# Performance work log

Hardware: AMD Instinct MI355X
Metric: run time of the kernel (lower is better)

## Reference

```python
import jax, jax.numpy as jnp
import numpy as np

B, N, F_IN, F_OUT = 8, 2048, 64, 64
ALPHA = 0.2
NEG = -9e15


def setup_inputs() -> dict:
    key = jax.random.key(0)
    k1, k2, k3, k4 = jax.random.split(key, 4)
    h = jax.random.normal(k1, (B, N, F_IN), dtype=jnp.float32)
    adj = jax.random.randint(k2, (N, N), 0, 2).astype(jnp.float32)
    W = jax.random.normal(k3, (F_OUT, F_IN), dtype=jnp.float32) * 0.05
    a = jax.random.normal(k4, (2 * F_OUT,), dtype=jnp.float32) * 0.05
    return {"h": h, "adj": adj, "W": W, "a": a}


def reference(h, adj, W, a):
    # Wh = h @ W^T  : [B, N, F_OUT]
    Wh = jnp.einsum("bnf,of->bno", h, W)
    # a([Wh_i, Wh_j]) decomposes exactly into a1.Wh_i + a2.Wh_j
    e1 = Wh @ a[:F_OUT]          # [B, N] contribution of source node i
    e2 = Wh @ a[F_OUT:]          # [B, N] contribution of target node j
    e = jax.nn.leaky_relu(e1[:, :, None] + e2[:, None, :], negative_slope=ALPHA)
    att = jnp.where(adj[None, :, :] > 0, e, NEG)
    att = jax.nn.softmax(att, axis=-1)   # [B, N, N]
    h_prime = jnp.einsum("bij,bjo->bio", att, Wh)
    return jax.nn.elu(h_prime)
```

## Files before the change

### kernel.cpp

```cpp
#include <hip/hip_runtime.h>
#include <hip/hip_bf16.h>
#include <math.h>


#define NN 2048
#define BB 8

typedef __attribute__((ext_vector_type(8))) short s8v;
typedef __attribute__((ext_vector_type(4))) float f4v;
typedef __attribute__((ext_vector_type(16))) float f16v;
typedef __attribute__((ext_vector_type(4))) unsigned u4v;

static __device__ __forceinline__ unsigned pk_bf16(float lo, float hi) {
  __hip_bfloat162 t = __float22bfloat162_rn(float2{lo, hi});
  return *(unsigned*)&t;
}
static __device__ __forceinline__ unsigned short bf16rne(float x) {
  union { float f; unsigned u; } c; c.f = x;
  unsigned r = c.u + 0x7FFFu + ((c.u >> 16) & 1u);
  return (unsigned short)(r >> 16);
}

__global__ __launch_bounds__(256, 2) void k_pre(
    const float* __restrict__ adj, const float* __restrict__ h,
    const float* __restrict__ W, const float* __restrict__ a,
    unsigned long long* __restrict__ adjq, unsigned short* __restrict__ whswz,
    float2* __restrict__ e1pn, unsigned* __restrict__ e2pk) {
  const int t = threadIdx.x, lane = t & 63, w = t >> 6;

  if (blockIdx.x >= 512) {
    const int bid = blockIdx.x - 512;
    const int row = bid * 2 + (w >> 1);
    const int half = w & 1;
    const float* ar = adj + (size_t)row * NN + half * 1024;
    unsigned long long* aq = adjq + row * 32 + half * 16;
    #pragma unroll
    for (int it = 0; it < 16; ++it) {
      unsigned long long m = __ballot(ar[it * 64 + lane] > 0.f);
      if (lane == 0) aq[it] = m;
    }
    return;
  }

  __shared__ __align__(16) float hs[32][68];
  const int rowBase = blockIdx.x * 32;
  const int b = rowBase >> 11, n0 = rowBase & (NN - 1);

  float wr[64];
  #pragma unroll
  for (int k = 0; k < 16; ++k)
    *(f4v*)&wr[k * 4] = *(const f4v*)&W[lane * 64 + k * 4];

  #pragma unroll
  for (int qq = 0; qq < 2; ++qq) {
    const int idx = t + 256 * qq;
    const int r = idx >> 4, c = (idx & 15) * 4;
    *(f4v*)&hs[r][c] = *(const f4v*)&h[(size_t)(rowBase + r) * 64 + c];
  }
  const float a1v = a[lane], a2v = a[64 + lane];
  __syncthreads();

  const int r0 = w * 8;
  float acc[8];
  #pragma unroll
  for (int rr = 0; rr < 8; ++rr) acc[rr] = 0.f;
  #pragma unroll
  for (int f4i = 0; f4i < 16; ++f4i) {
    f4v hv[8];
    #pragma unroll
    for (int rr = 0; rr < 8; ++rr)
      hv[rr] = *(const f4v*)&hs[r0 + rr][f4i * 4];
    #pragma unroll
    for (int x = 0; x < 4; ++x) {
      const float wv = wr[f4i * 4 + x];
      #pragma unroll
      for (int rr = 0; rr < 8; ++rr) acc[rr] = fmaf(hv[rr][x], wv, acc[rr]);
    }
  }

  {
    union { s8v v; unsigned u[4]; } cv;
    cv.u[0] = pk_bf16(acc[0], acc[1]);
    cv.u[1] = pk_bf16(acc[2], acc[3]);
    cv.u[2] = pk_bf16(acc[4], acc[5]);
    cv.u[3] = pk_bf16(acc[6], acc[7]);
    const int jc = (n0 + w * 8) >> 4;
    const int oh = lane >> 5;
    const int lp = ((w & 1) << 5) + (lane & 31);
    unsigned short* dst = whswz + ((size_t)b << 17) + (jc << 10) + (oh << 9) + (lp << 3);
    *(s8v*)dst = cv.v;
  }

  float s1[8], s2[8];
  #pragma unroll
  for (int rr = 0; rr < 8; ++rr) { s1[rr] = acc[rr] * a1v; s2[rr] = acc[rr] * a2v; }
  #pragma unroll
  for (int m = 1; m < 64; m <<= 1)
    #pragma unroll
    for (int rr = 0; rr < 8; ++rr) {
      s1[rr] += __shfl_xor(s1[rr], m);
      s2[rr] += __shfl_xor(s2[rr], m);
    }
  #pragma unroll
  for (int rr = 0; rr < 8; ++rr) {
    if (lane == 0) {
      e1pn[rowBase + rr + r0] = float2{__expf(s1[rr]), __expf(0.2f * s1[rr])};
      e2pk[rowBase + rr + r0] =
          (unsigned)bf16rne(__expf(s2[rr])) |
          ((unsigned)bf16rne(__expf(0.2f * s2[rr])) << 16);
    }
  }
}

__global__ __launch_bounds__(512, 4) void k_attn(
    const unsigned long long* __restrict__ adjq,
    const unsigned short* __restrict__ whswz,
    const float2* __restrict__ e1png, const unsigned* __restrict__ e2pkg,
    float* __restrict__ out) {
  union SM {
    unsigned e2bf[NN];
    float pc[8][32][68];
  };
  __shared__ __align__(16) SM sm;
  __shared__ float ls[8][32];

  const int t = threadIdx.x, lane = t & 63, w = t >> 6;
  const int m32 = lane & 31, kh = lane >> 5;
  const int g = blockIdx.x;
  const int b = g & 7;
  const int i0 = (g >> 3) << 5;
  const size_t bN = (size_t)b * NN;

  ((u4v*)sm.e2bf)[t] = ((const u4v*)(e2pkg + bN))[t];

  const float2 e1f = e1png[bN + i0 + m32];
  const float E1p = e1f.x, E1n = e1f.y;
  const unsigned long long* arow = adjq + (size_t)(i0 + m32) * 32 + w * 4;
  const unsigned short* wb = whswz + ((size_t)b << 17);

  f16v acc0, acc1;
  #pragma unroll
  for (int r = 0; r < 16; ++r) { acc0[r] = 0.f; acc1[r] = 0.f; }
  float psum = 0.f;

  auto pgen = [&](u4v e0, u4v e1, unsigned bits) -> s8v {
    float p[8];
    #pragma unroll
    for (int e = 0; e < 8; ++e) {
      const unsigned dw = e < 4 ? e0[e] : e1[e - 4];
      const float E2p = __uint_as_float(dw << 16);
      const float E2n = __uint_as_float(dw & 0xffff0000u);
      const float mp = E1p * E2p;
      const float mn = E1n * E2n;
      float pv = mp > 1.f ? mp : mn;
      pv = ((bits >> e) & 1u) ? pv : 0.f;
      psum += pv;
      p[e] = pv;
    }
    union { s8v v; unsigned u[4]; } cv;
    cv.u[0] = pk_bf16(p[0], p[1]);
    cv.u[1] = pk_bf16(p[2], p[3]);
    cv.u[2] = pk_bf16(p[4], p[5]);
    cv.u[3] = pk_bf16(p[6], p[7]);
    return cv.v;
  };

  __syncthreads();

  unsigned long long am = 0;
  #pragma unroll
  for (int it = 0; it < 8; ++it) {
    const int jcl = it * 2;
    const int jcA = w * 16 + jcl, jcB = jcA + 1;
    const s8v bA0 = *(const s8v*)(wb + (jcA << 10) + (lane << 3));
    const s8v bA1 = *(const s8v*)(wb + (jcA << 10) + 512 + (lane << 3));
    const s8v bB0 = *(const s8v*)(wb + (jcB << 10) + (lane << 3));
    const s8v bB1 = *(const s8v*)(wb + (jcB << 10) + 512 + (lane << 3));
    if ((it & 1) == 0) am = arow[it >> 1];
    const u4v eA0 = *(const u4v*)&sm.e2bf[(jcA << 4) + (kh << 3)];
    const u4v eA1 = *(const u4v*)&sm.e2bf[(jcA << 4) + (kh << 3) + 4];
    const u4v eB0 = *(const u4v*)&sm.e2bf[(jcB << 4) + (kh << 3)];
    const u4v eB1 = *(const u4v*)&sm.e2bf[(jcB << 4) + (kh << 3) + 4];

    const unsigned bitsA = (unsigned)(am >> (((jcl)&3) * 16 + kh * 8)) & 0xffu;
    const unsigned bitsB = (unsigned)(am >> (((jcl + 1) & 3) * 16 + kh * 8)) & 0xffu;
    const s8v afA = pgen(eA0, eA1, bitsA);
    const s8v afB = pgen(eB0, eB1, bitsB);

    acc0 = __builtin_amdgcn_mfma_f32_32x32x16_bf16(afA, bA0, acc0, 0, 0, 0);
    acc1 = __builtin_amdgcn_mfma_f32_32x32x16_bf16(afA, bA1, acc1, 0, 0, 0);
    acc0 = __builtin_amdgcn_mfma_f32_32x32x16_bf16(afB, bB0, acc0, 0, 0, 0);
    acc1 = __builtin_amdgcn_mfma_f32_32x32x16_bf16(afB, bB1, acc1, 0, 0, 0);
  }

  psum += __shfl_xor(psum, 32);
  __syncthreads();
  if (lane < 32) ls[w][lane] = psum;
  #pragma unroll
  for (int r = 0; r < 16; ++r) {
    const int row = (r & 3) + 8 * (r >> 2) + 4 * kh;
    sm.pc[w][row][m32] = acc0[r];
    sm.pc[w][row][32 + m32] = acc1[r];
  }
  __syncthreads();

  const int row = t >> 4, c0 = (t & 15) * 4;
  f4v sum = *(const f4v*)&sm.pc[0][row][c0];
  #pragma unroll
  for (int j = 1; j < 8; ++j) sum += *(const f4v*)&sm.pc[j][row][c0];
  float rsum = ls[0][row];
  #pragma unroll
  for (int j = 1; j < 8; ++j) rsum += ls[j][row];
  f4v o;
  #pragma unroll
  for (int x = 0; x < 4; ++x) {
    float v = sum[x] / rsum;
    o[x] = v > 0.f ? v : expm1f(v);
  }
  *(f4v*)&out[(bN + i0 + row) * 64 + c0] = o;
}

extern "C" void kernel_launch(void* const* d_in, const int* in_sizes, int n_in,
                              void* d_out, int out_size, void* d_ws, size_t ws_size,
                              hipStream_t stream) {
  (void)in_sizes; (void)n_in; (void)out_size; (void)ws_size;
  const float* h   = (const float*)d_in[0];
  const float* adj = (const float*)d_in[1];
  const float* W   = (const float*)d_in[2];
  const float* a   = (const float*)d_in[3];
  float* outp = (float*)d_out;

  unsigned short* whswz = (unsigned short*)d_ws;
  float2* e1pn = (float2*)((char*)d_ws + (size_t)BB * 64 * NN * 2);
  unsigned* e2pk = (unsigned*)(e1pn + (size_t)BB * NN);
  unsigned long long* adjq = (unsigned long long*)(e2pk + (size_t)BB * NN);

  k_pre<<<1536, 256, 0, stream>>>(adj, h, W, a, adjq, whswz, e1pn, e2pk);
  k_attn<<<512, 512, 0, stream>>>(adjq, whswz, e1pn, e2pk, outp);
}
```

Baseline: 97.88 us.

## Halve attention block to 4 waves with 4-deep prefetched Wh ring

The attention kernel now runs 4 waves per block instead of 8, so each wave handles 32 j-chunks instead of 16. The wave loads all its adjacency bits up front and keeps Wh tiles in a 4-stage register ring, issuing each global load four iterations before the matching MFMA. It also splits the row-sum into two accumulators and shrinks the cross-wave reduction buffer. The cost is half as many threads in flight per block, more registers per wave and a longer serial loop per wave.

```diff
diff --git a/kernel.cpp b/kernel.cpp
--- a/kernel.cpp
+++ b/kernel.cpp
@@ -10,6 +10,7 @@
 typedef __attribute__((ext_vector_type(4))) float f4v;
 typedef __attribute__((ext_vector_type(16))) float f16v;
 typedef __attribute__((ext_vector_type(4))) unsigned u4v;
+typedef __attribute__((ext_vector_type(2))) unsigned long long u64v2;
 
 static __device__ __forceinline__ unsigned pk_bf16(float lo, float hi) {
   __hip_bfloat162 t = __float22bfloat162_rn(float2{lo, hi});
@@ -112,17 +113,17 @@
   }
 }
 
-__global__ __launch_bounds__(512, 4) void k_attn(
+__global__ __launch_bounds__(256, 2) void k_attn(
     const unsigned long long* __restrict__ adjq,
     const unsigned short* __restrict__ whswz,
     const float2* __restrict__ e1png, const unsigned* __restrict__ e2pkg,
     float* __restrict__ out) {
   union SM {
     unsigned e2bf[NN];
-    float pc[8][32][68];
+    float pc[4][32][68];
   };
   __shared__ __align__(16) SM sm;
-  __shared__ float ls[8][32];
+  __shared__ float ls[4][32];
 
   const int t = threadIdx.x, lane = t & 63, w = t >> 6;
   const int m32 = lane & 31, kh = lane >> 5;
@@ -132,18 +133,40 @@
   const size_t bN = (size_t)b * NN;
 
   ((u4v*)sm.e2bf)[t] = ((const u4v*)(e2pkg + bN))[t];
+  ((u4v*)sm.e2bf)[t + 256] = ((const u4v*)(e2pkg + bN))[t + 256];
 
   const float2 e1f = e1png[bN + i0 + m32];
   const float E1p = e1f.x, E1n = e1f.y;
-  const unsigned long long* arow = adjq + (size_t)(i0 + m32) * 32 + w * 4;
-  const unsigned short* wb = whswz + ((size_t)b << 17);
+
+  const unsigned long long* arow = adjq + (size_t)(i0 + m32) * 32 + w * 8;
+  unsigned long long am[8];
+  #pragma unroll
+  for (int qq = 0; qq < 4; ++qq)
+    *(u64v2*)&am[qq * 2] = *(const u64v2*)(arow + qq * 2);
+
+  const unsigned short* wb = whswz + ((size_t)b << 17) + ((size_t)(w * 32) << 10);
 
   f16v acc0, acc1;
   #pragma unroll
   for (int r = 0; r < 16; ++r) { acc0[r] = 0.f; acc1[r] = 0.f; }
-  float psum = 0.f;
-
-  auto pgen = [&](u4v e0, u4v e1, unsigned bits) -> s8v {
+  float psA = 0.f, psB = 0.f;
+
+  s8v buf[4][2];
+  #pragma unroll
+  for (int k = 0; k < 4; ++k) {
+    buf[k][0] = *(const s8v*)(wb + (k << 10) + (lane << 3));
+    buf[k][1] = *(const s8v*)(wb + (k << 10) + 512 + (lane << 3));
+  }
+
+  __syncthreads();
+
+  #pragma unroll 4
+  for (int k = 0; k < 32; ++k) {
+    const int x = k & 3;
+    const int eb = ((w * 32 + k) << 4) + (kh << 3);
+    const u4v e0 = *(const u4v*)&sm.e2bf[eb];
+    const u4v e1 = *(const u4v*)&sm.e2bf[eb + 4];
+    const unsigned bits = (unsigned)(am[k >> 2] >> ((k & 3) * 16 + kh * 8)) & 0xffu;
     float p[8];
     #pragma unroll
     for (int e = 0; e < 8; ++e) {
@@ -154,45 +177,34 @@
       const float mn = E1n * E2n;
       float pv = mp > 1.f ? mp : mn;
       pv = ((bits >> e) & 1u) ? pv : 0.f;
-      psum += pv;
       p[e] = pv;
     }
-    union { s8v v; unsigned u[4]; } cv;
-    cv.u[0] = pk_bf16(p[0], p[1]);
-    cv.u[1] = pk_bf16(p[2], p[3]);
-    cv.u[2] = pk_bf16(p[4], p[5]);
-    cv.u[3] = pk_bf16(p[6], p[7]);
-    return cv.v;
-  };
-
-  __syncthreads();
-
-  unsigned long long am = 0;
-  #pragma unroll
-  for (int it = 0; it < 8; ++it) {
-    const int jcl = it * 2;
-    const int jcA = w * 16 + jcl, jcB = jcA + 1;
-    const s8v bA0 = *(const s8v*)(wb + (jcA << 10) + (lane << 3));
-    const s8v bA1 = *(const s8v*)(wb + (jcA << 10) + 512 + (lane << 3));
-    const s8v bB0 = *(const s8v*)(wb + (jcB << 10) + (lane << 3));
-    const s8v bB1 = *(const s8v*)(wb + (jcB << 10) + 512 + (lane << 3));
-    if ((it & 1) == 0) am = arow[it >> 1];
-    const u4v eA0 = *(const u4v*)&sm.e2bf[(jcA << 4) + (kh << 3)];
-    const u4v eA1 = *(const u4v*)&sm.e2bf[(jcA << 4) + (kh << 3) + 4];
-    const u4v eB0 = *(const u4v*)&sm.e2bf[(jcB << 4) + (kh << 3)];
-    const u4v eB1 = *(const u4v*)&sm.e2bf[(jcB << 4) + (kh << 3) + 4];
-
-    const unsigned bitsA = (unsigned)(am >> (((jcl)&3) * 16 + kh * 8)) & 0xffu;
-    const unsigned bitsB = (unsigned)(am >> (((jcl + 1) & 3) * 16 + kh * 8)) & 0xffu;
-    const s8v afA = pgen(eA0, eA1, bitsA);
-    const s8v afB = pgen(eB0, eB1, bitsB);
-
-    acc0 = __builtin_amdgcn_mfma_f32_32x32x16_bf16(afA, bA0, acc0, 0, 0, 0);
-    acc1 = __builtin_amdgcn_mfma_f32_32x32x16_bf16(afA, bA1, acc1, 0, 0, 0);
-    acc0 = __builtin_amdgcn_mfma_f32_32x32x16_bf16(afB, bB0, acc0, 0, 0, 0);
-    acc1 = __builtin_amdgcn_mfma_f32_32x32x16_bf16(afB, bB1, acc1, 0, 0, 0);
-  }
-
+    {
+      const float s01 = p[0] + p[1], s23 = p[2] + p[3];
+      const float s45 = p[4] + p[5], s67 = p[6] + p[7];
+      if (k & 1) psB += (s01 + s23) + (s45 + s67);
+      else       psA += (s01 + s23) + (s45 + s67);
+    }
+    s8v af;
+    {
+      union { s8v v; unsigned u[4]; } cv;
+      cv.u[0] = pk_bf16(p[0], p[1]);
+      cv.u[1] = pk_bf16(p[2], p[3]);
+      cv.u[2] = pk_bf16(p[4], p[5]);
+      cv.u[3] = pk_bf16(p[6], p[7]);
+      af = cv.v;
+    }
+
+    acc0 = __builtin_amdgcn_mfma_f32_32x32x16_bf16(af, buf[x][0], acc0, 0, 0, 0);
+    acc1 = __builtin_amdgcn_mfma_f32_32x32x16_bf16(af, buf[x][1], acc1, 0, 0, 0);
+
+    if (k < 28) {
+      buf[x][0] = *(const s8v*)(wb + ((k + 4) << 10) + (lane << 3));
+      buf[x][1] = *(const s8v*)(wb + ((k + 4) << 10) + 512 + (lane << 3));
+    }
+  }
+
+  float psum = psA + psB;
   psum += __shfl_xor(psum, 32);
   __syncthreads();
   if (lane < 32) ls[w][lane] = psum;
@@ -204,20 +216,26 @@
   }
   __syncthreads();
 
-  const int row = t >> 4, c0 = (t & 15) * 4;
-  f4v sum = *(const f4v*)&sm.pc[0][row][c0];
-  #pragma unroll
-  for (int j = 1; j < 8; ++j) sum += *(const f4v*)&sm.pc[j][row][c0];
-  float rsum = ls[0][row];
-  #pragma unroll
-  for (int j = 1; j < 8; ++j) rsum += ls[j][row];
-  f4v o;
-  #pragma unroll
-  for (int x = 0; x < 4; ++x) {
-    float v = sum[x] / rsum;
-    o[x] = v > 0.f ? v : expm1f(v);
-  }
-  *(f4v*)&out[(bN + i0 + row) * 64 + c0] = o;
+  const int row = t >> 3, c0 = (t & 7) * 8;
+  f4v s0 = *(const f4v*)&sm.pc[0][row][c0];
+  f4v s1 = *(const f4v*)&sm.pc[0][row][c0 + 4];
+  #pragma unroll
+  for (int j = 1; j < 4; ++j) {
+    s0 += *(const f4v*)&sm.pc[j][row][c0];
+    s1 += *(const f4v*)&sm.pc[j][row][c0 + 4];
+  }
+  const float rsum = ls[0][row] + ls[1][row] + ls[2][row] + ls[3][row];
+  f4v o0, o1;
+  #pragma unroll
+  for (int xx = 0; xx < 4; ++xx) {
+    float v = s0[xx] / rsum;
+    o0[xx] = v > 0.f ? v : expm1f(v);
+    v = s1[xx] / rsum;
+    o1[xx] = v > 0.f ? v : expm1f(v);
+  }
+  float* op = &out[(bN + i0 + row) * 64 + c0];
+  *(f4v*)op = o0;
+  *(f4v*)(op + 4) = o1;
 }
 
 extern "C" void kernel_launch(void* const* d_in, const int* in_sizes, int n_in,
@@ -236,5 +254,5 @@
   unsigned long long* adjq = (unsigned long long*)(e2pk + (size_t)BB * NN);
 
   k_pre<<<1536, 256, 0, stream>>>(adj, h, W, a, adjq, whswz, e1pn, e2pk);
-  k_attn<<<512, 512, 0, stream>>>(adjq, whswz, e1pn, e2pk, outp);
-}
+  k_attn<<<512, 256, 0, stream>>>(adjq, whswz, e1pn, e2pk, outp);
+}
```

New measurement: 100.4 us. 2.6% more time.
